# Performance work log

Hardware: AMD Instinct MI355X
Metric: run time of the kernel (lower is better)

## Reference

```python
import jax, jax.numpy as jnp
import numpy as np

B, C, H, W = 16, 512, 24, 24


def setup_inputs() -> dict:
    key = jax.random.key(0)
    ks = jax.random.split(key, 7)
    s = 0.02
    return {
        "x5": jax.random.normal(ks[0], (B, C, H, W), jnp.float32),
        "conv_w": jax.random.normal(ks[1], (C, C), jnp.float32) * s,
        "conv_b": jax.random.normal(ks[2], (C,), jnp.float32) * s,
        "q_w": jax.random.normal(ks[3], (C, C), jnp.float32) * s,
        "q_b": jax.random.normal(ks[4], (C,), jnp.float32) * s,
        "k_w": jax.random.normal(ks[5], (C, C), jnp.float32) * s,
        "k_b": jax.random.normal(ks[6], (C,), jnp.float32) * s,
    }


def _conv1x1(x, w, b):
    # 1x1 conv == channel matmul: (O,C) x (B,C,H,W) -> (B,O,H,W)
    return jnp.einsum('oc,bchw->bohw', w, x) + b[None, :, None, None]


def reference(x5, conv_w, conv_b, q_w, q_b, k_w, k_b):
    Bb, Cc, Hh, Ww = x5.shape
    scale = 1.0 / (Cc ** 0.5)
    x5 = _conv1x1(x5, conv_w, conv_b) + x5
    # my_SS2D source was not provided in the module; treated as identity (see notes)
    x00 = x5
    # cross-batch correlation: queries (B*H*W, C), keys (B, C, H*W)
    q = _conv1x1(x00, q_w, q_b).reshape(Bb, Cc, Hh * Ww).transpose(0, 2, 1).reshape(Bb * Hh * Ww, Cc)
    k = _conv1x1(x00, k_w, k_b).reshape(Bb, Cc, Hh * Ww)
    # scores: (B*H*W, B, H*W); max over locations, mean over images
    scores = jnp.einsum('nc,bcm->nbm', q, k) * scale
    x_w = scores.max(axis=-1).mean(axis=-1).reshape(Bb, Hh * Ww)
    x_w = jax.nn.softmax(x_w, axis=-1)
    # channel-wise L2 normalize (F.normalize, eps=1e-12)
    nrm = jnp.sqrt(jnp.sum(x5 * x5, axis=1, keepdims=True))
    norm0 = x5 / jnp.maximum(nrm, 1e-12)
    # top-1 (equality-based) seed mask per image
    x_w_max = x_w.max(axis=-1, keepdims=True)
    mask = (x_w == x_w_max).astype(x5.dtype).reshape(Bb, 1, Hh, Ww)
    seeds = (norm0 * mask).sum(axis=(2, 3))  # (B, C)
    # seeded 1x1-conv correlation (eval mode -> relu): (B, B_seeds, H, W)
    corr = jax.nn.relu(jnp.einsum('bchw,sc->bshw', norm0, seeds)).mean(axis=1).reshape(Bb, Hh * Ww)
    mn = corr.min(axis=-1, keepdims=True)
    mx = corr.max(axis=-1, keepdims=True)
    cormap = ((corr - mn) / (mx - mn + 1e-12)).reshape(Bb, 1, Hh, Ww)
    x51 = x5 * cormap
    proto1 = jnp.mean(x51, axis=(0, 2, 3), keepdims=True)  # (1, C, 1, 1)
    return (x5, proto1, x5 * proto1 + x51, mask)
```

## Files before the change

### kernel.cpp

```cpp
#include <hip/hip_runtime.h>
#include <math.h>

#define BB   16
#define CC   512
#define HWW  576
#define NN   9216
#define CHW  (CC*HWW)
#define TOT  (BB*CHW)
#define SCALE 0.044194173824159216f
#define FRAGB 9437184

typedef __attribute__((ext_vector_type(8))) __bf16 bf16x8;
typedef __attribute__((ext_vector_type(4))) float f32x4;

#define AS1 __attribute__((address_space(1)))
#define AS3 __attribute__((address_space(3)))

static __device__ __forceinline__ void gload_lds16(const void* g, void* l)
{
    __builtin_amdgcn_global_load_lds((AS1 const void*)g, (AS3 void*)l, 16, 0, 0);
}


__global__ __launch_bounds__(256)
void prep_x_kernel(const float* __restrict__ X, __bf16* __restrict__ Xhi,
                   __bf16* __restrict__ Xlo)
{
    int g = blockIdx.x * 256 + threadIdx.x;
    int n = g % NN;
    int co = g / NN;
    int c0 = co * 8;
    int bimg = n / HWW, mm = n % HWW;
    const float* src = X + (size_t)bimg * CHW + mm;
    union { __bf16 h[8]; float4 f4; } uh, ul;
#pragma unroll
    for (int j = 0; j < 8; j++) {
        float v = src[(size_t)(c0 + j) * HWW];
        __bf16 h = (__bf16)v;
        uh.h[j] = h;
        ul.h[j] = (__bf16)(v - (float)h);
    }
    int Cb = c0 >> 6, s = (c0 >> 5) & 1, q8 = (c0 >> 3) & 3;
    int T = n >> 6, g4 = (n >> 4) & 3, Lm = n & 15;
    size_t off = (size_t)(Cb * 144 + T) * 4096 + (s * 4 + g4) * 512 + (size_t)((q8 << 4) | Lm) * 8;
    *(float4*)&Xhi[off] = uh.f4;
    *(float4*)&Xlo[off] = ul.f4;
}

__global__ __launch_bounds__(256)
void prep_w_kernel(const float* __restrict__ cw, const float* __restrict__ qw,
                   const float* __restrict__ kw, __bf16* __restrict__ cwhi,
                   __bf16* __restrict__ cwlo, __bf16* __restrict__ qwf,
                   __bf16* __restrict__ kwf)
{
    int y = blockIdx.y;
    const float* W = (y == 0) ? cw : (y == 1) ? qw : kw;
    __bf16* dh = (y == 0) ? cwhi : (y == 1) ? qwf : kwf;
    int g = blockIdx.x * 256 + threadIdx.x;
    int o = g >> 6;
    int c0 = (g & 63) * 8;
    union { __bf16 h[8]; float4 f4; } uh, ul;
#pragma unroll
    for (int j = 0; j < 8; j++) {
        float v = W[(size_t)o * CC + c0 + j];
        __bf16 h = (__bf16)v;
        uh.h[j] = h;
        ul.h[j] = (__bf16)(v - (float)h);
    }
    int Cb = c0 >> 6, s = (c0 >> 5) & 1, q8 = (c0 >> 3) & 3;
    int To = o >> 6, g4 = (o >> 4) & 3, Lm = o & 15;
    size_t off = (size_t)(Cb * 8 + To) * 4096 + (s * 4 + g4) * 512 + (size_t)((q8 << 4) | Lm) * 8;
    *(float4*)&dh[off] = uh.f4;
    if (y == 0) *(float4*)&cwlo[off] = ul.f4;
}

__global__ __launch_bounds__(256)
void conv1_mfma_kernel(const float* __restrict__ X, const __bf16* __restrict__ Whi,
                       const __bf16* __restrict__ Wlo, const __bf16* __restrict__ Xhi,
                       const __bf16* __restrict__ Xlo, const float* __restrict__ bias,
                       float* __restrict__ Y, __bf16* __restrict__ Yfrag)
{
    __shared__ __bf16 lAh[8192], lAl[8192], lBh[8192], lBl[8192];
    int tid = threadIdx.x, lane = tid & 63, wv = tid >> 6;
    int wo = wv >> 1, wm = wv & 1;
    int m0 = blockIdx.x * 128;
    int o0 = blockIdx.y * 128;
    int oT0 = blockIdx.y * 2, mT0 = blockIdx.x * 2;

    f32x4 acc[4][4];
#pragma unroll
    for (int i = 0; i < 4; i++)
#pragma unroll
        for (int j = 0; j < 4; j++) acc[i][j] = (f32x4){0.f, 0.f, 0.f, 0.f};

    for (int Cb = 0; Cb < 8; Cb++) {
        const float4* gAh = (const float4*)(Whi + (size_t)(Cb * 8 + oT0) * 4096);
        const float4* gAl = (const float4*)(Wlo + (size_t)(Cb * 8 + oT0) * 4096);
        const float4* gBh = (const float4*)(Xhi + (size_t)(Cb * 144 + mT0) * 4096);
        const float4* gBl = (const float4*)(Xlo + (size_t)(Cb * 144 + mT0) * 4096);
#pragma unroll
        for (int i = 0; i < 4; i++) {
            int eb = wv * 256 + i * 64;
            gload_lds16(gAh + eb + lane, (float4*)lAh + eb);
            gload_lds16(gAl + eb + lane, (float4*)lAl + eb);
            gload_lds16(gBh + eb + lane, (float4*)lBh + eb);
            gload_lds16(gBl + eb + lane, (float4*)lBl + eb);
        }
        __syncthreads();
#pragma unroll
        for (int s = 0; s < 2; s++) {
            bf16x8 ah[4], al[4], bh[4], bl[4];
#pragma unroll
            for (int ga = 0; ga < 4; ga++) {
                ah[ga] = *(const bf16x8*)&lAh[wo * 4096 + (s * 4 + ga) * 512 + lane * 8];
                al[ga] = *(const bf16x8*)&lAl[wo * 4096 + (s * 4 + ga) * 512 + lane * 8];
            }
#pragma unroll
            for (int gb = 0; gb < 4; gb++) {
                bh[gb] = *(const bf16x8*)&lBh[wm * 4096 + (s * 4 + gb) * 512 + lane * 8];
                bl[gb] = *(const bf16x8*)&lBl[wm * 4096 + (s * 4 + gb) * 512 + lane * 8];
            }
#pragma unroll
            for (int ga = 0; ga < 4; ga++)
#pragma unroll
                for (int gb = 0; gb < 4; gb++) {
                    acc[ga][gb] = __builtin_amdgcn_mfma_f32_16x16x32_bf16(ah[ga], bh[gb], acc[ga][gb], 0, 0, 0);
                    acc[ga][gb] = __builtin_amdgcn_mfma_f32_16x16x32_bf16(ah[ga], bl[gb], acc[ga][gb], 0, 0, 0);
                    acc[ga][gb] = __builtin_amdgcn_mfma_f32_16x16x32_bf16(al[ga], bh[gb], acc[ga][gb], 0, 0, 0);
                }
        }
        __syncthreads();
    }

    int quad = lane >> 4, col = lane & 15;
#pragma unroll
    for (int ga = 0; ga < 4; ga++) {
        int ob = o0 + wo * 64 + ga * 16 + quad * 4;
        float bs[4];
#pragma unroll
        for (int r = 0; r < 4; r++) bs[r] = bias[ob + r];
        int Cb2 = ob >> 6, s2 = (ob >> 5) & 1, q8 = (ob >> 3) & 3, j0 = ob & 7;
#pragma unroll
        for (int gb = 0; gb < 4; gb++) {
            int n = m0 + wm * 64 + gb * 16 + col;
            int T = n >> 6, g4 = (n >> 4) & 3, Lm = n & 15;
            int bimg = n / HWW, mm = n % HWW;
            size_t xb = (size_t)bimg * CHW + mm;
            union { __bf16 h[4]; float2 f2; } u;
#pragma unroll
            for (int r = 0; r < 4; r++) {
                float v = acc[ga][gb][r] + bs[r] + X[xb + (size_t)(ob + r) * HWW];
                Y[xb + (size_t)(ob + r) * HWW] = v;
                u.h[r] = (__bf16)v;
            }
            *(float2*)&Yfrag[(size_t)(Cb2 * 144 + T) * 4096 + (s2 * 4 + g4) * 512 + (size_t)((q8 << 4) | Lm) * 8 + j0] = u.f2;
        }
    }
}

__global__ __launch_bounds__(256)
void convqk_mfma_kernel(const __bf16* __restrict__ qwf, const __bf16* __restrict__ kwf,
                        const float* __restrict__ qb, const float* __restrict__ kb,
                        const __bf16* __restrict__ Xf, __bf16* __restrict__ Oq,
                        __bf16* __restrict__ Ok)
{
    const __bf16* Wf = blockIdx.z ? kwf : qwf;
    const float* bias = blockIdx.z ? kb : qb;
    __bf16* Of = blockIdx.z ? Ok : Oq;

    __shared__ __bf16 lA[8192], lB[8192];
    int tid = threadIdx.x, lane = tid & 63, wv = tid >> 6;
    int wo = wv >> 1, wm = wv & 1;
    int m0 = blockIdx.x * 128;
    int o0 = blockIdx.y * 128;
    int oT0 = blockIdx.y * 2, mT0 = blockIdx.x * 2;

    f32x4 acc[4][4];
#pragma unroll
    for (int i = 0; i < 4; i++)
#pragma unroll
        for (int j = 0; j < 4; j++) acc[i][j] = (f32x4){0.f, 0.f, 0.f, 0.f};

    for (int Cb = 0; Cb < 8; Cb++) {
        const float4* gA = (const float4*)(Wf + (size_t)(Cb * 8 + oT0) * 4096);
        const float4* gB = (const float4*)(Xf + (size_t)(Cb * 144 + mT0) * 4096);
#pragma unroll
        for (int i = 0; i < 4; i++) {
            int eb = wv * 256 + i * 64;
            gload_lds16(gA + eb + lane, (float4*)lA + eb);
            gload_lds16(gB + eb + lane, (float4*)lB + eb);
        }
        __syncthreads();
#pragma unroll
        for (int s = 0; s < 2; s++) {
            bf16x8 af[4], bf[4];
#pragma unroll
            for (int ga = 0; ga < 4; ga++)
                af[ga] = *(const bf16x8*)&lA[wo * 4096 + (s * 4 + ga) * 512 + lane * 8];
#pragma unroll
            for (int gb = 0; gb < 4; gb++)
                bf[gb] = *(const bf16x8*)&lB[wm * 4096 + (s * 4 + gb) * 512 + lane * 8];
#pragma unroll
            for (int ga = 0; ga < 4; ga++)
#pragma unroll
                for (int gb = 0; gb < 4; gb++)
                    acc[ga][gb] = __builtin_amdgcn_mfma_f32_16x16x32_bf16(af[ga], bf[gb], acc[ga][gb], 0, 0, 0);
        }
        __syncthreads();
    }

    int quad = lane >> 4, col = lane & 15;
#pragma unroll
    for (int ga = 0; ga < 4; ga++) {
        int ob = o0 + wo * 64 + ga * 16 + quad * 4;
        float bs[4];
#pragma unroll
        for (int r = 0; r < 4; r++) bs[r] = bias[ob + r];
        int Cb2 = ob >> 6, s2 = (ob >> 5) & 1, q8 = (ob >> 3) & 3, j0 = ob & 7;
#pragma unroll
        for (int gb = 0; gb < 4; gb++) {
            int n = m0 + wm * 64 + gb * 16 + col;
            int T = n >> 6, g4 = (n >> 4) & 3, Lm = n & 15;
            union { __bf16 h[4]; float2 f2; } u;
#pragma unroll
            for (int r = 0; r < 4; r++) u.h[r] = (__bf16)(acc[ga][gb][r] + bs[r]);
            *(float2*)&Of[(size_t)(Cb2 * 144 + T) * 4096 + (s2 * 4 + g4) * 512 + (size_t)((q8 << 4) | Lm) * 8 + j0] = u.f2;
        }
    }
}

__global__ __launch_bounds__(256)
void scores_mfma_kernel(const __bf16* __restrict__ Qf, const __bf16* __restrict__ Kf,
                        float* __restrict__ maxv3)
{
    __shared__ __bf16 ldsQ[8192];
    __shared__ __bf16 ldsK[12288];

    int tid = threadIdx.x, lane = tid & 63, wv = tid >> 6;
    int wq = wv >> 1, wk = wv & 1;
    int bx = blockIdx.x;
    int n0 = bx * 128;
    int b = blockIdx.y / 3, mt = blockIdx.y % 3;

    f32x4 acc[4][6];
#pragma unroll
    for (int ga = 0; ga < 4; ga++)
#pragma unroll
        for (int t = 0; t < 6; t++) acc[ga][t] = (f32x4){0.f, 0.f, 0.f, 0.f};

    const __bf16* qbase = Qf + (size_t)(bx * 2) * 4096;
    const __bf16* kbase = Kf + (size_t)(b * 9 + mt * 3) * 4096;

    for (int C = 0; C < 8; C++) {
        const float4* gq = (const float4*)(qbase + (size_t)C * 144 * 4096);
        const float4* gk = (const float4*)(kbase + (size_t)C * 144 * 4096);
#pragma unroll
        for (int i = 0; i < 4; i++) {
            int eb = wv * 256 + i * 64;
            gload_lds16(gq + eb + lane, (float4*)ldsQ + eb);
        }
#pragma unroll
        for (int i = 0; i < 6; i++) {
            int eb = wv * 384 + i * 64;
            gload_lds16(gk + eb + lane, (float4*)ldsK + eb);
        }
        __syncthreads();
#pragma unroll
        for (int s = 0; s < 2; s++) {
            bf16x8 af[4];
#pragma unroll
            for (int ga = 0; ga < 4; ga++)
                af[ga] = *(const bf16x8*)&ldsQ[wq * 4096 + (s * 4 + ga) * 512 + lane * 8];
#pragma unroll
            for (int t = 0; t < 6; t++) {
                int mkl = wk * 96 + t * 16;
                bf16x8 bfr = *(const bf16x8*)&ldsK[(mkl >> 6) * 4096 + (s * 4 + ((mkl >> 4) & 3)) * 512 + lane * 8];
#pragma unroll
                for (int ga = 0; ga < 4; ga++)
                    acc[ga][t] = __builtin_amdgcn_mfma_f32_16x16x32_bf16(af[ga], bfr, acc[ga][t], 0, 0, 0);
            }
        }
        __syncthreads();
    }

    float mg[4][4];
#pragma unroll
    for (int ga = 0; ga < 4; ga++)
#pragma unroll
        for (int r = 0; r < 4; r++) {
            float v = acc[ga][0][r];
#pragma unroll
            for (int t = 1; t < 6; t++) v = fmaxf(v, acc[ga][t][r]);
            mg[ga][r] = v;
        }
#pragma unroll
    for (int off = 1; off < 16; off <<= 1)
#pragma unroll
        for (int ga = 0; ga < 4; ga++)
#pragma unroll
            for (int r = 0; r < 4; r++)
                mg[ga][r] = fmaxf(mg[ga][r], __shfl_xor(mg[ga][r], off, 64));

    float (*redbuf)[2] = (float (*)[2])ldsQ;
    if ((lane & 15) == 0) {
        int quad = lane >> 4;
#pragma unroll
        for (int ga = 0; ga < 4; ga++)
#pragma unroll
            for (int r = 0; r < 4; r++)
                redbuf[wq * 64 + ga * 16 + quad * 4 + r][wk] = mg[ga][r];
    }
    __syncthreads();
    if (tid < 128) {
        float rv = fmaxf(redbuf[tid][0], redbuf[tid][1]) * SCALE;
        maxv3[((size_t)(n0 + tid) * BB + b) * 3 + mt] = rv;
    }
}

__global__ __launch_bounds__(576)
void topk_kernel(const float* __restrict__ maxv3, int* __restrict__ cand)
{
    __shared__ float sv[576];
    __shared__ float rv_[64];
    __shared__ int ri_[64];
    int bi = blockIdx.x, m = threadIdx.x;
    int n = bi * HWW + m;
    float v = 0.f;
#pragma unroll
    for (int t = 0; t < BB; t++) {
        const float* p = maxv3 + ((size_t)n * BB + t) * 3;
        v += fmaxf(fmaxf(p[0], p[1]), p[2]);
    }
    sv[m] = v;
    __syncthreads();
    for (int r = 0; r < 4; r++) {
        if (m < 64) {
            float bv = sv[m]; int bidx = m;
            for (int j = m + 64; j < 576; j += 64)
                if (sv[j] > bv) { bv = sv[j]; bidx = j; }
            rv_[m] = bv; ri_[m] = bidx;
        }
        __syncthreads();
        if (m == 0) {
            float bv = rv_[0]; int bidx = ri_[0];
            for (int j = 1; j < 64; j++)
                if (rv_[j] > bv) { bv = rv_[j]; bidx = ri_[j]; }
            cand[bi * 4 + r] = bidx;
            sv[bidx] = -3.4e38f;
        }
        __syncthreads();
    }
}

__global__ __launch_bounds__(256)
void refine_q_kernel(const float* __restrict__ x5, const float* __restrict__ qw,
                     const float* __restrict__ qb, const int* __restrict__ cand,
                     float* __restrict__ q_all)
{
    int og = blockIdx.x, cd = blockIdx.y;
    int bi = cd >> 2;
    int mstar = cand[cd];
    int tid = threadIdx.x, w = tid >> 6, lane = tid & 63;
    __shared__ float xcol[512];
    __shared__ float qrows[64];
    xcol[tid]       = x5[(size_t)bi * CHW + tid * HWW + mstar];
    xcol[tid + 256] = x5[(size_t)bi * CHW + (tid + 256) * HWW + mstar];
    __syncthreads();
#pragma unroll
    for (int i = 0; i < 16; i++) {
        int r = og * 64 + w * 16 + i;
        float p = 0.f;
#pragma unroll
        for (int it = 0; it < 8; it++) {
            int c = lane + it * 64;
            p = fmaf(qw[(size_t)r * 512 + c], xcol[c], p);
        }
        for (int off = 32; off; off >>= 1) p += __shfl_down(p, off, 64);
        if (lane == 0) qrows[w * 16 + i] = p;
    }
    __syncthreads();
    if (tid < 64) q_all[(size_t)cd * 512 + og * 64 + tid] = qrows[tid] + qb[og * 64 + tid];
}

__global__ __launch_bounds__(256)
void refine_u2_kernel(const float* __restrict__ kw, const float* __restrict__ kb,
                      const float* __restrict__ q_all, float* __restrict__ u_all,
                      float* __restrict__ qkbg)
{
    int tg = blockIdx.x, cd = blockIdx.y;
    int tid = threadIdx.x;
    __shared__ float qs[512];
    qs[tid]       = q_all[(size_t)cd * 512 + tid];
    qs[tid + 256] = q_all[(size_t)cd * 512 + tid + 256];
    __syncthreads();
    int t = tg * 256 + tid;
    float u = 0.f;
    for (int o = 0; o < 512; o++)
        u = fmaf(kw[(size_t)o * 512 + t], qs[o], u);
    u_all[(size_t)cd * 512 + t] = u;
    if (tg == 0) {
        float pk = qs[tid] * kb[tid] + qs[tid + 256] * kb[tid + 256];
        for (int off = 32; off; off >>= 1) pk += __shfl_down(pk, off, 64);
        __shared__ float pr[4];
        if ((tid & 63) == 0) pr[tid >> 6] = pk;
        __syncthreads();
        if (tid == 0) qkbg[cd] = pr[0] + pr[1] + pr[2] + pr[3];
    }
}

__global__ __launch_bounds__(256)
void refine_max_kernel(const float* __restrict__ x5, const float* __restrict__ u_all,
                       float* __restrict__ maxex9)
{
    int bp = blockIdx.x, cg = blockIdx.y, mc = blockIdx.z;
    int tid = threadIdx.x, mi = tid & 63, cs = tid >> 6;
    int m0 = mc * 64;
    __shared__ float us[16 * 512];
    __shared__ float red[256];
    for (int e = tid; e < 16 * 512; e += 256) us[e] = u_all[(size_t)cg * 16 * 512 + e];
    __syncthreads();

    float acc[16];
#pragma unroll
    for (int j = 0; j < 16; j++) acc[j] = 0.f;
    const float* xb = x5 + (size_t)bp * CHW + m0 + mi;
    for (int cc = 0; cc < 128; cc++) {
        int c = cs * 128 + cc;
        float x = xb[(size_t)c * HWW];
#pragma unroll
        for (int j = 0; j < 16; j++)
            acc[j] = fmaf(us[j * 512 + c], x, acc[j]);
    }

#pragma unroll
    for (int j = 0; j < 16; j++) {
        red[tid] = acc[j];
        __syncthreads();
        if (tid < 64) {
            float v = red[tid] + red[tid + 64] + red[tid + 128] + red[tid + 192];
            for (int off = 32; off; off >>= 1) v = fmaxf(v, __shfl_xor(v, off, 64));
            if (tid == 0) maxex9[((size_t)(cg * 16 + j) * BB + bp) * 9 + mc] = v;
        }
        __syncthreads();
    }
}

__global__ __launch_bounds__(576)
void mask_kernel(const float* __restrict__ maxex9, const float* __restrict__ qkbg,
                 const int* __restrict__ cand, float* __restrict__ maskout)
{
    int bi = blockIdx.x, m = threadIdx.x;
    __shared__ float ve[4];
    __shared__ int chosen;
    if (m < 4) {
        int cd = bi * 4 + m;
        float sacc = 0.f;
#pragma unroll
        for (int t = 0; t < BB; t++) {
            const float* p = maxex9 + ((size_t)cd * BB + t) * 9;
            float mv = p[0];
#pragma unroll
            for (int z = 1; z < 9; z++) mv = fmaxf(mv, p[z]);
            sacc += mv;
        }
        ve[m] = sacc * (1.f / 16.f) + qkbg[cd];
    }
    __syncthreads();
    if (m == 0) {
        int best = 0; float bv = ve[0];
        for (int j = 1; j < 4; j++) if (ve[j] > bv) { bv = ve[j]; best = j; }
        chosen = cand[bi * 4 + best];
    }
    __syncthreads();
    maskout[bi * HWW + m] = (m == chosen) ? 1.f : 0.f;
}

__global__ __launch_bounds__(256)
void norm_kernel(const float* __restrict__ X5, float* __restrict__ invb)
{
    int b = blockIdx.y;
    int m0 = blockIdx.x * 64;
    int mi = threadIdx.x & 63, cs = threadIdx.x >> 6;
    float s = 0.f;
    for (int c = cs; c < CC; c += 4) {
        float x = X5[b * CHW + c * HWW + m0 + mi];
        s = fmaf(x, x, s);
    }
    __shared__ float red[4][64];
    red[cs][mi] = s;
    __syncthreads();
    if (cs == 0) {
        float t = red[0][mi] + red[1][mi] + red[2][mi] + red[3][mi];
        invb[b * HWW + m0 + mi] = 1.0f / fmaxf(sqrtf(t), 1e-12f);
    }
}

__global__ __launch_bounds__(256)
void seeds_kernel(const float* __restrict__ X5, const float* __restrict__ invb,
                  const float* __restrict__ maskf, float* __restrict__ seeds)
{
    int s = blockIdx.y;
    int c = blockIdx.x * 4 + (threadIdx.x >> 6);
    int mi = threadIdx.x & 63;
    float acc = 0.f;
    for (int mt = 0; mt < 9; mt++) {
        int m = mt * 64 + mi;
        float w = invb[s * HWW + m] * maskf[s * HWW + m];
        acc = fmaf(X5[s * CHW + c * HWW + m], w, acc);
    }
    for (int off = 32; off > 0; off >>= 1) acc += __shfl_down(acc, off, 64);
    if (mi == 0) seeds[s * CC + c] = acc;
}

__global__ __launch_bounds__(256)
void corr_kernel(const float* __restrict__ X5, const float* __restrict__ invb,
                 const float* __restrict__ seeds, float* __restrict__ corr)
{
    __shared__ float sd[16 * 512];
    __shared__ float xs[64][65];
    __shared__ float red[4][64];
    int b = blockIdx.y;
    int m0 = blockIdx.x * 64;
    int tid = threadIdx.x;
    int mi = tid & 63, sg = tid >> 6;

    for (int e = tid; e < 16 * 512; e += 256) sd[e] = seeds[e];

    float acc[4] = {0.f, 0.f, 0.f, 0.f};
    for (int c0 = 0; c0 < CC; c0 += 64) {
        __syncthreads();
        for (int e = tid; e < 4096; e += 256) {
            int mm = e & 63, kk = e >> 6;
            xs[kk][mm] = X5[b * CHW + (c0 + kk) * HWW + m0 + mm];
        }
        __syncthreads();
#pragma unroll
        for (int kk = 0; kk < 64; kk++) {
            float xv = xs[kk][mi];
#pragma unroll
            for (int t = 0; t < 4; t++)
                acc[t] = fmaf(xv, sd[(sg * 4 + t) * CC + c0 + kk], acc[t]);
        }
    }
    float r = 0.f;
#pragma unroll
    for (int t = 0; t < 4; t++) r += fmaxf(acc[t], 0.f);
    red[sg][mi] = r;
    __syncthreads();
    if (sg == 0) {
        float tot = red[0][mi] + red[1][mi] + red[2][mi] + red[3][mi];
        corr[b * HWW + m0 + mi] = invb[b * HWW + m0 + mi] * tot * (1.0f / 16.0f);
    }
}

__global__ __launch_bounds__(576)
void cormap_kernel(const float* __restrict__ corr, float* __restrict__ cormap)
{
    __shared__ float sv[576];
    __shared__ float smn[64], smx[64];
    __shared__ float s_mn, s_mx;
    int b = blockIdx.x;
    int m = threadIdx.x;
    float v = corr[b * HWW + m];
    sv[m] = v;
    __syncthreads();
    if (m < 64) {
        float mn = sv[m], mx = sv[m];
        for (int j = m + 64; j < 576; j += 64) { mn = fminf(mn, sv[j]); mx = fmaxf(mx, sv[j]); }
        smn[m] = mn; smx[m] = mx;
    }
    __syncthreads();
    if (m == 0) {
        float mn = smn[0], mx = smx[0];
        for (int j = 1; j < 64; j++) { mn = fminf(mn, smn[j]); mx = fmaxf(mx, smx[j]); }
        s_mn = mn; s_mx = mx;
    }
    __syncthreads();
    cormap[b * HWW + m] = (v - s_mn) / (s_mx - s_mn + 1e-12f);
}

__global__ __launch_bounds__(256)
void proto_kernel(const float* __restrict__ X5, const float* __restrict__ cormap,
                  float* __restrict__ proto1)
{
    int c = blockIdx.x;
    int tid = threadIdx.x;
    float acc = 0.f;
    for (int p = tid; p < NN; p += 256) {
        int b = p / HWW, m = p % HWW;
        acc = fmaf(X5[b * CHW + c * HWW + m], cormap[p], acc);
    }
    for (int off = 32; off > 0; off >>= 1) acc += __shfl_down(acc, off, 64);
    __shared__ float red[4];
    if ((tid & 63) == 0) red[tid >> 6] = acc;
    __syncthreads();
    if (tid == 0) proto1[c] = (red[0] + red[1] + red[2] + red[3]) * (1.0f / (float)NN);
}

__global__ __launch_bounds__(256)
void final_kernel(const float* __restrict__ X5, const float* __restrict__ proto1,
                  const float* __restrict__ cormap, float* __restrict__ out3)
{
    int idx = blockIdx.x * 256 + threadIdx.x;
    if (idx >= TOT) return;
    int b = idx / CHW;
    int r = idx % CHW;
    int c = r / HWW;
    int m = r % HWW;
    float x = X5[idx];
    out3[idx] = x * (proto1[c] + cormap[b * HWW + m]);
}

extern "C" void kernel_launch(void* const* d_in, const int* in_sizes, int n_in,
                              void* d_out, int out_size, void* d_ws, size_t ws_size,
                              hipStream_t stream)
{
    const float* x  = (const float*)d_in[0];
    const float* cw = (const float*)d_in[1];
    const float* cb = (const float*)d_in[2];
    const float* qw = (const float*)d_in[3];
    const float* qb = (const float*)d_in[4];
    const float* kw = (const float*)d_in[5];
    const float* kb = (const float*)d_in[6];

    float* out     = (float*)d_out;
    float* x5o     = out;
    float* proto1  = out + TOT;
    float* out3    = out + TOT + 512;
    float* maskout = out + TOT + 512 + TOT;

    char* o3 = (char*)out3;
    __bf16* xlo    = (__bf16*)o3;
    __bf16* qfrag  = (__bf16*)o3;
    __bf16* x5frag = (__bf16*)(o3 + FRAGB);

    char* ws = (char*)d_ws;
    __bf16* xhi   = (__bf16*)ws;
    __bf16* kfrag = (__bf16*)ws;
    __bf16* cwhi  = (__bf16*)(ws + FRAGB);
    __bf16* cwlo  = (__bf16*)(ws + FRAGB + 524288);
    __bf16* qwf   = (__bf16*)(ws + FRAGB + 2 * 524288);
    __bf16* kwf   = (__bf16*)(ws + FRAGB + 3 * 524288);
    char* p = ws + FRAGB + 4 * 524288;
    float* maxv3  = (float*)p;   p += (size_t)NN * BB * 3 * 4;
    int*   cand   = (int*)p;     p += 256;
    float* q_all  = (float*)p;   p += 64 * 512 * 4;
    float* u_all  = (float*)p;   p += 64 * 512 * 4;
    float* qkbg   = (float*)p;   p += 256;
    float* maxex9 = (float*)p;   p += 64 * BB * 9 * 4;
    float* invb   = (float*)p;   p += NN * 4;
    float* corr   = (float*)p;   p += NN * 4;
    float* cmap   = (float*)p;   p += NN * 4;
    float* seeds  = (float*)p;   p += BB * CC * 4;

    prep_x_kernel<<<NN * 64 / 256, 256, 0, stream>>>(x, xhi, xlo);
    prep_w_kernel<<<dim3(128, 3), 256, 0, stream>>>(cw, qw, kw, cwhi, cwlo, qwf, kwf);

    conv1_mfma_kernel<<<dim3(NN / 128, 4), 256, 0, stream>>>(x, cwhi, cwlo, xhi, xlo, cb, x5o, x5frag);
    convqk_mfma_kernel<<<dim3(NN / 128, 4, 2), 256, 0, stream>>>(qwf, kwf, qb, kb, x5frag, qfrag, kfrag);

    scores_mfma_kernel<<<dim3(NN / 128, BB * 3), 256, 0, stream>>>(qfrag, kfrag, maxv3);

    topk_kernel<<<BB, HWW, 0, stream>>>(maxv3, cand);
    refine_q_kernel<<<dim3(8, 64), 256, 0, stream>>>(x5o, qw, qb, cand, q_all);
    refine_u2_kernel<<<dim3(2, 64), 256, 0, stream>>>(kw, kb, q_all, u_all, qkbg);
    refine_max_kernel<<<dim3(BB, 4, 9), 256, 0, stream>>>(x5o, u_all, maxex9);
    mask_kernel<<<BB, HWW, 0, stream>>>(maxex9, qkbg, cand, maskout);

    norm_kernel<<<dim3(9, BB), 256, 0, stream>>>(x5o, invb);
    seeds_kernel<<<dim3(CC / 4, BB), 256, 0, stream>>>(x5o, invb, maskout, seeds);
    corr_kernel<<<dim3(9, BB), 256, 0, stream>>>(x5o, invb, seeds, corr);
    cormap_kernel<<<BB, HWW, 0, stream>>>(corr, cmap);
    proto_kernel<<<CC, 256, 0, stream>>>(x5o, cmap, proto1);
    final_kernel<<<(TOT + 255) / 256, 256, 0, stream>>>(x5o, proto1, cmap, out3);
}
```

Measured before the change: 376.6 us.

## Gather seeds directly from chosen index and simplify tail kernels' indexing

The seeds kernel now reads a single column at the index chosen by the mask kernel, which writes that index out, instead of reducing over all locations with a mask. refine_max batches its 16 reductions behind one barrier, using a larger shared buffer. proto and final kernels drop per-element div/mod by using per-(b,c) row loops. These trim small tail kernels. They do not touch the dominant MFMA stages. Seeds match the old path only when the mask has one nonzero; on exact ties in the top-1 the results differ.

```diff
diff --git a/kernel.cpp b/kernel.cpp
--- a/kernel.cpp
+++ b/kernel.cpp
@@ -416,7 +416,7 @@
     int tid = threadIdx.x, mi = tid & 63, cs = tid >> 6;
     int m0 = mc * 64;
     __shared__ float us[16 * 512];
-    __shared__ float red[256];
+    __shared__ float red[16][4][64];
     for (int e = tid; e < 16 * 512; e += 256) us[e] = u_all[(size_t)cg * 16 * 512 + e];
     __syncthreads();
 
@@ -431,23 +431,23 @@
         for (int j = 0; j < 16; j++)
             acc[j] = fmaf(us[j * 512 + c], x, acc[j]);
     }
-
-#pragma unroll
-    for (int j = 0; j < 16; j++) {
-        red[tid] = acc[j];
-        __syncthreads();
-        if (tid < 64) {
-            float v = red[tid] + red[tid + 64] + red[tid + 128] + red[tid + 192];
+#pragma unroll
+    for (int j = 0; j < 16; j++) red[j][cs][mi] = acc[j];
+    __syncthreads();
+    if (tid < 64) {
+#pragma unroll
+        for (int j = 0; j < 16; j++) {
+            float v = red[j][0][tid] + red[j][1][tid] + red[j][2][tid] + red[j][3][tid];
             for (int off = 32; off; off >>= 1) v = fmaxf(v, __shfl_xor(v, off, 64));
-            if (tid == 0) maxex9[((size_t)(cg * 16 + j) * BB + bp) * 9 + mc] = v;
-        }
-        __syncthreads();
+            if (tid == j) maxex9[((size_t)(cg * 16 + j) * BB + bp) * 9 + mc] = v;
+        }
     }
 }
 
 __global__ __launch_bounds__(576)
 void mask_kernel(const float* __restrict__ maxex9, const float* __restrict__ qkbg,
-                 const int* __restrict__ cand, float* __restrict__ maskout)
+                 const int* __restrict__ cand, float* __restrict__ maskout,
+                 int* __restrict__ chosenidx)
 {
     int bi = blockIdx.x, m = threadIdx.x;
     __shared__ float ve[4];
@@ -470,6 +470,7 @@
         int best = 0; float bv = ve[0];
         for (int j = 1; j < 4; j++) if (ve[j] > bv) { bv = ve[j]; best = j; }
         chosen = cand[bi * 4 + best];
+        chosenidx[bi] = chosen;
     }
     __syncthreads();
     maskout[bi * HWW + m] = (m == chosen) ? 1.f : 0.f;
@@ -495,21 +496,14 @@
     }
 }
 
-__global__ __launch_bounds__(256)
-void seeds_kernel(const float* __restrict__ X5, const float* __restrict__ invb,
-                  const float* __restrict__ maskf, float* __restrict__ seeds)
-{
-    int s = blockIdx.y;
-    int c = blockIdx.x * 4 + (threadIdx.x >> 6);
-    int mi = threadIdx.x & 63;
-    float acc = 0.f;
-    for (int mt = 0; mt < 9; mt++) {
-        int m = mt * 64 + mi;
-        float w = invb[s * HWW + m] * maskf[s * HWW + m];
-        acc = fmaf(X5[s * CHW + c * HWW + m], w, acc);
-    }
-    for (int off = 32; off > 0; off >>= 1) acc += __shfl_down(acc, off, 64);
-    if (mi == 0) seeds[s * CC + c] = acc;
+__global__ __launch_bounds__(512)
+void seeds_direct_kernel(const float* __restrict__ X5, const float* __restrict__ invb,
+                         const int* __restrict__ chosenidx, float* __restrict__ seeds)
+{
+    int s = blockIdx.x, c = threadIdx.x;
+    int mstar = chosenidx[s];
+    float w = invb[s * HWW + mstar];
+    seeds[s * CC + c] = X5[(size_t)s * CHW + (size_t)c * HWW + mstar] * w;
 }
 
 __global__ __launch_bounds__(256)
@@ -586,9 +580,11 @@
     int c = blockIdx.x;
     int tid = threadIdx.x;
     float acc = 0.f;
-    for (int p = tid; p < NN; p += 256) {
-        int b = p / HWW, m = p % HWW;
-        acc = fmaf(X5[b * CHW + c * HWW + m], cormap[p], acc);
+    for (int b = 0; b < BB; b++) {
+        const float* xp = X5 + (size_t)b * CHW + (size_t)c * HWW;
+        const float* cp = cormap + b * HWW;
+        for (int m = tid; m < HWW; m += 256)
+            acc = fmaf(xp[m], cp[m], acc);
     }
     for (int off = 32; off > 0; off >>= 1) acc += __shfl_down(acc, off, 64);
     __shared__ float red[4];
@@ -597,18 +593,19 @@
     if (tid == 0) proto1[c] = (red[0] + red[1] + red[2] + red[3]) * (1.0f / (float)NN);
 }
 
-__global__ __launch_bounds__(256)
+__global__ __launch_bounds__(192)
 void final_kernel(const float* __restrict__ X5, const float* __restrict__ proto1,
                   const float* __restrict__ cormap, float* __restrict__ out3)
 {
-    int idx = blockIdx.x * 256 + threadIdx.x;
-    if (idx >= TOT) return;
-    int b = idx / CHW;
-    int r = idx % CHW;
-    int c = r / HWW;
-    int m = r % HWW;
-    float x = X5[idx];
-    out3[idx] = x * (proto1[c] + cormap[b * HWW + m]);
+    int c = blockIdx.x, b = blockIdx.y;
+    size_t base = (size_t)b * CHW + (size_t)c * HWW;
+    float pc = proto1[c];
+    const float* cp = cormap + b * HWW;
+#pragma unroll
+    for (int k = 0; k < 3; k++) {
+        int m = threadIdx.x + k * 192;
+        out3[base + m] = X5[base + m] * (pc + cp[m]);
+    }
 }
 
 extern "C" void kernel_launch(void* const* d_in, const int* in_sizes, int n_in,
@@ -644,6 +641,7 @@
     char* p = ws + FRAGB + 4 * 524288;
     float* maxv3  = (float*)p;   p += (size_t)NN * BB * 3 * 4;
     int*   cand   = (int*)p;     p += 256;
+    int*   chosenidx = (int*)p;  p += 256;
     float* q_all  = (float*)p;   p += 64 * 512 * 4;
     float* u_all  = (float*)p;   p += 64 * 512 * 4;
     float* qkbg   = (float*)p;   p += 256;
@@ -665,12 +663,12 @@
     refine_q_kernel<<<dim3(8, 64), 256, 0, stream>>>(x5o, qw, qb, cand, q_all);
     refine_u2_kernel<<<dim3(2, 64), 256, 0, stream>>>(kw, kb, q_all, u_all, qkbg);
     refine_max_kernel<<<dim3(BB, 4, 9), 256, 0, stream>>>(x5o, u_all, maxex9);
-    mask_kernel<<<BB, HWW, 0, stream>>>(maxex9, qkbg, cand, maskout);
+    mask_kernel<<<BB, HWW, 0, stream>>>(maxex9, qkbg, cand, maskout, chosenidx);
 
     norm_kernel<<<dim3(9, BB), 256, 0, stream>>>(x5o, invb);
-    seeds_kernel<<<dim3(CC / 4, BB), 256, 0, stream>>>(x5o, invb, maskout, seeds);
+    seeds_direct_kernel<<<BB, 512, 0, stream>>>(x5o, invb, chosenidx, seeds);
     corr_kernel<<<dim3(9, BB), 256, 0, stream>>>(x5o, invb, seeds, corr);
     cormap_kernel<<<BB, HWW, 0, stream>>>(corr, cmap);
     proto_kernel<<<CC, 256, 0, stream>>>(x5o, cmap, proto1);
-    final_kernel<<<(TOT + 255) / 256, 256, 0, stream>>>(x5o, proto1, cmap, out3);
-}
+    final_kernel<<<dim3(CC, BB), 192, 0, stream>>>(x5o, proto1, cmap, out3);
+}
```

New measurement: 371.2 us. No clear change (-1.4%).
